# Performance work log

Hardware: AMD Instinct MI355X
Metric: run time of the kernel (lower is better)

## Reference

```python
import jax, jax.numpy as jnp
import numpy as np

EMB = 1024   # emb_dim
HID = 1024   # hid_dim (must equal EMB for the original router to be well-formed)
E = 16       # num_experts
K = 2        # num_active_experts


def setup_inputs() -> dict:
    key = jax.random.key(0)
    ks = jax.random.split(key, 5)
    s_in = (2.0 / EMB) ** 0.5
    s_hid = (2.0 / HID) ** 0.5
    x = jax.random.normal(ks[0], (2, 4096, EMB), dtype=jnp.float32)
    w_gate = jax.random.normal(ks[1], (EMB, E), dtype=jnp.float32) * s_in
    w1 = jax.random.normal(ks[2], (E, EMB, HID), dtype=jnp.float32) * s_in  # exp_1 weights
    w2 = jax.random.normal(ks[3], (E, EMB, HID), dtype=jnp.float32) * s_in  # exp_2 weights
    wc = jax.random.normal(ks[4], (E, HID, EMB), dtype=jnp.float32) * s_hid  # contr weights
    return {"x": x, "w_gate": w_gate, "w1": w1, "w2": w2, "wc": wc}


def reference(x, w_gate, w1, w2, wc):
    b, s, d = x.shape
    xf = x.reshape(-1, d)                      # [N, d]
    n = xf.shape[0]
    # Router: softmax over expert logits, then top-k (no renormalization of topk scores,
    # matching the torch module).
    probs = jax.nn.softmax(xf @ w_gate, axis=-1)   # [N, E]
    scores, idx = jax.lax.top_k(probs, K)          # [N, K]
    # Dense gate matrix: gate[t, e] = score if e in topk(t) else 0 (topk indices distinct).
    gates = jnp.zeros((n, E), dtype=xf.dtype).at[jnp.arange(n)[:, None], idx].set(scores)
    # Loop (scan) over the fixed expert count; each expert runs a SwiGLU MLP over all
    # tokens and its output is combined with the (mostly zero) gate weights. This is the
    # standard dense-combine MoE reference: same math as the masked torch loop since
    # unselected tokens get gate 0.
    def body(acc, ws):
        w1e, w2e, wce, ge = ws                 # [d,h], [d,h], [h,d], [N]
        h = jax.nn.silu(xf @ w1e) * (xf @ w2e)  # [N, h]
        return acc + ge[:, None] * (h @ wce), None

    out, _ = jax.lax.scan(body, jnp.zeros_like(xf), (w1, w2, wc, gates.T))
    return out.reshape(b, s, d)
```

## Files before the change

kernel.cpp:

```cpp
#include <hip/hip_runtime.h>
#include <hip/hip_bf16.h>
#include <stdint.h>

#define EMB 1024
#define HID 1024
#define NE 16
#define NTOK 8192
#define NSLOT (NTOK * 2)
#define BM 128
#define BN 128
#define BK 32

typedef __bf16 bf16;
typedef __bf16 bf16x8 __attribute__((ext_vector_type(8)));
typedef __bf16 bf16x4 __attribute__((ext_vector_type(4)));
typedef float f32x4 __attribute__((ext_vector_type(4)));

#define GLOAD16(g, l)                                                        \
  __builtin_amdgcn_global_load_lds(                                          \
      (const __attribute__((address_space(1))) void*)(g),                    \
      (__attribute__((address_space(3))) void*)(l), 16, 0, 0)

#define VMW(N) asm volatile("s_waitcnt vmcnt(" #N ")" ::: "memory")
#define NOPS ((void)0)

#define PH_PRE                                                \
  __builtin_amdgcn_s_barrier();                               \
  __builtin_amdgcn_s_setprio(1)
#define PH_POST                                               \
  __builtin_amdgcn_s_setprio(0);                              \
  __builtin_amdgcn_s_barrier()

#define LDA2(D, M, CK) (*(const bf16x8*)&sh[((((D)<<1) + wm) << 13) + l15 * 64 + (CK) + (M) * 1024])
#define LDB2(D, N, CK) (*(const bf16x8*)&sh[32768 + ((((D)<<1) + (wn >> 1)) << 13) + ((wn & 1) << 12) + l15 * 64 + (CK) + (N) * 1024])

#define STG2_A(D, KO) do {                                                    \
    GLOAD16(agp00 + (KO), (char*)sh + ((((D)<<1) + 0) << 14) + wb);           \
    GLOAD16(agp01 + (KO), (char*)sh + ((((D)<<1) + 0) << 14) + 8192 + wb);    \
    GLOAD16(agp10 + (KO), (char*)sh + ((((D)<<1) + 1) << 14) + wb);           \
    GLOAD16(agp11 + (KO), (char*)sh + ((((D)<<1) + 1) << 14) + 8192 + wb);    \
  } while (0)
#define STG2_B(D, KO) do {                                                    \
    GLOAD16(bgp00 + (KO), (char*)sh + 65536 + ((((D)<<1) + 0) << 14) + wb);   \
    GLOAD16(bgp01 + (KO), (char*)sh + 65536 + ((((D)<<1) + 0) << 14) + 8192 + wb); \
    GLOAD16(bgp10 + (KO), (char*)sh + 65536 + ((((D)<<1) + 1) << 14) + wb);   \
    GLOAD16(bgp11 + (KO), (char*)sh + 65536 + ((((D)<<1) + 1) << 14) + 8192 + wb); \
  } while (0)

#define MM(MB, FA, FB) do {                                                   \
    _Pragma("unroll") for (int mq = 0; mq < 4; mq++)                          \
    _Pragma("unroll") for (int nq = 0; nq < 4; nq++)                          \
      acc[(MB) + mq][nq] = __builtin_amdgcn_mfma_f32_16x16x32_bf16(           \
          (FA)[mq], (FB)[nq], acc[(MB) + mq][nq], 0, 0, 0);                   \
  } while (0)

#define KTILE2(D, S2, W2) do {                                                \
    bf16x8 a0[8], b0[4];                                                      \
    _Pragma("unroll") for (int q = 0; q < 4; q++) b0[q] = LDB2(D, q, c0);     \
    _Pragma("unroll") for (int q = 0; q < 8; q++) a0[q] = LDA2(D, q, c0);     \
    PH_PRE; MM(0, a0, b0); MM(4, a0 + 4, b0); PH_POST;                        \
    bf16x8 a1[8], b1[4];                                                      \
    _Pragma("unroll") for (int q = 0; q < 4; q++) b1[q] = LDB2(D, q, c1);     \
    _Pragma("unroll") for (int q = 0; q < 8; q++) a1[q] = LDA2(D, q, c1);     \
    S2; W2;                                                                   \
    PH_PRE; MM(0, a1, b1); MM(4, a1 + 4, b1); PH_POST;                        \
  } while (0)

#define KLOOP2(NT2) do {                                                      \
    STG2_A(0, 0); STG2_B(0, 0); STG2_A(1, 64); STG2_B(1, 64);                 \
    VMW(8); __builtin_amdgcn_s_barrier();                                     \
    _Pragma("unroll 1") for (int i = 0; i < (NT2) - 1; i++) {                 \
      int k2 = (i * 2 + 2) * 64, k3 = (i * 2 + 3) * 64;                       \
      KTILE2(0, { STG2_B(0, k2); STG2_A(0, k2); }, VMW(8));                   \
      KTILE2(1, { STG2_B(1, k3); STG2_A(1, k3); }, VMW(8));                   \
    }                                                                         \
    KTILE2(0, NOPS, VMW(0));                                                  \
    KTILE2(1, NOPS, NOPS);                                                    \
  } while (0)

__global__ void wgT_k(const float* __restrict__ wg, float* __restrict__ wgT) {
  int f = blockIdx.x * 256 + threadIdx.x;
  int d = f >> 4, e = f & 15;
  wgT[e * 1024 + d] = wg[f];
}

__launch_bounds__(512)
__global__ void prep_k(const float* __restrict__ w1, const float* __restrict__ w2,
                       const float* __restrict__ wcs, bf16* __restrict__ w1t,
                       bf16* __restrict__ w2t, bf16* __restrict__ wct,
                       const float* __restrict__ x, const float* __restrict__ wgT,
                       bf16* __restrict__ xb,
                       int* __restrict__ tokexp, float* __restrict__ tokgate) {
  __shared__ __align__(16) char lds[65536];
  int bid = blockIdx.x;
  if (bid < 6144) {
    typedef bf16 TileT[64][68];
    TileT* tile = (TileT*)lds;
    int half = threadIdx.x >> 8, t = threadIdx.x & 255;
    int u = bid * 2 + half;
    int zz = u >> 8, t16 = u & 255;
    int n0 = (t16 & 15) << 6, k0 = (t16 >> 4) << 6;
    const float* s; bf16* d;
    if (zz < 16)      { s = w1;  d = w1t; }
    else if (zz < 32) { s = w2;  d = w2t; }
    else              { s = wcs; d = wct; }
    int z = zz & 15;
    s += (size_t)z << 20;
    d += (size_t)z << 20;

    int r = t >> 4, c4 = t & 15;
#pragma unroll
    for (int i = 0; i < 4; i++) {
      int row = r + (i << 4);
      float4 v = *(const float4*)&s[(size_t)(k0 + row) * 1024 + n0 + (c4 << 2)];
      bf16x4 o;
      o[0] = (bf16)v.x; o[1] = (bf16)v.y; o[2] = (bf16)v.z; o[3] = (bf16)v.w;
      *(bf16x4*)&tile[half][row][c4 << 2] = o;
    }
    __syncthreads();

    int r8 = t >> 3, ch = t & 7;
#pragma unroll
    for (int i = 0; i < 2; i++) {
      int on = r8 + (i << 5);
      bf16x8 v;
#pragma unroll
      for (int j = 0; j < 8; j++) v[j] = tile[half][(ch << 3) + j][on];
      *(bf16x8*)&d[(size_t)(n0 + on) * 1024 + k0 + (ch << 3)] = v;
    }
  } else {
    float* wgs = (float*)lds;
    for (int i = threadIdx.x; i < 4096; i += 512)
      ((float4*)wgs)[i] = ((const float4*)wgT)[i];
    __syncthreads();

    int tok = (bid - 6144) * 8 + (threadIdx.x >> 6);
    int lane = threadIdx.x & 63;
    const float* xr = x + (size_t)tok * EMB;

    float acc[NE];
#pragma unroll
    for (int e = 0; e < NE; e++) acc[e] = 0.f;

#pragma unroll
    for (int c = 0; c < 4; c++) {
      float4 xv = ((const float4*)xr)[c * 64 + lane];
      int dbase = c * 256 + lane * 4;
      bf16x4 o;
      o[0] = (bf16)xv.x; o[1] = (bf16)xv.y; o[2] = (bf16)xv.z; o[3] = (bf16)xv.w;
      *(bf16x4*)(xb + (size_t)tok * EMB + dbase) = o;
#pragma unroll
      for (int e = 0; e < NE; e++) {
        float4 wv = *(const float4*)&wgs[e * 1024 + dbase];
        acc[e] += xv.x * wv.x + xv.y * wv.y + xv.z * wv.z + xv.w * wv.w;
      }
    }
#pragma unroll
    for (int e = 0; e < NE; e++) {
#pragma unroll
      for (int s2 = 32; s2 > 0; s2 >>= 1) acc[e] += __shfl_xor(acc[e], s2);
    }
    if (lane == 0) {
      float m = acc[0];
#pragma unroll
      for (int e = 1; e < NE; e++) m = fmaxf(m, acc[e]);
      float p[NE]; float sum = 0.f;
#pragma unroll
      for (int e = 0; e < NE; e++) { p[e] = __expf(acc[e] - m); sum += p[e]; }
      float inv = 1.f / sum;
#pragma unroll
      for (int e = 0; e < NE; e++) p[e] *= inv;
      int i1 = 0;
#pragma unroll
      for (int e = 1; e < NE; e++) if (p[e] > p[i1]) i1 = e;
      int i2 = (i1 == 0) ? 1 : 0;
#pragma unroll
      for (int e = 0; e < NE; e++) if (e != i1 && p[e] > p[i2]) i2 = e;
      tokexp[2 * tok] = i1; tokexp[2 * tok + 1] = i2;
      tokgate[2 * tok] = p[i1]; tokgate[2 * tok + 1] = p[i2];
    }
  }
}

__global__ void hist_k(const int* __restrict__ tokexp, int* __restrict__ blockcnt) {
  __shared__ int h[NE];
  int tid = threadIdx.x;
  if (tid < NE) h[tid] = 0;
  __syncthreads();
  int e = tokexp[blockIdx.x * 256 + tid];
  atomicAdd(&h[e], 1);
  __syncthreads();
  if (tid < NE) blockcnt[blockIdx.x * NE + tid] = h[tid];
}

__global__ void scan_k(const int* __restrict__ blockcnt, int* __restrict__ cnt,
                       int* __restrict__ eoff, int* __restrict__ blockoff) {
  __shared__ int scnt[NE], soff[NE];
  int t = threadIdx.x;
  if (t < NE) {
    int s = 0;
    for (int b = 0; b < 64; b++) s += blockcnt[b * NE + t];
    scnt[t] = s;
    cnt[t] = s;
  }
  __syncthreads();
  if (t == 0) {
    int s = 0;
    for (int e = 0; e < NE; e++) { soff[e] = s; eoff[e] = s; s += scnt[e]; }
  }
  __syncthreads();
  if (t < NE) {
    int run = soff[t];
    for (int b = 0; b < 64; b++) { blockoff[b * NE + t] = run; run += blockcnt[b * NE + t]; }
  }
}

__global__ void assign_k(const int* __restrict__ tokexp, const float* __restrict__ tokgate,
                         const int* __restrict__ blockoff, int* __restrict__ rowtok,
                         float* __restrict__ rowgate, int* __restrict__ posof) {
  __shared__ int wavecnt[4][NE];
  __shared__ int waveoff[4][NE];
  int tid = threadIdx.x;
  int w = tid >> 6, lane = tid & 63;
  int s = blockIdx.x * 256 + tid;
  int e = tokexp[s];
  int rank = 0;
  unsigned long long ltmask = (1ull << lane) - 1ull;
#pragma unroll
  for (int ee = 0; ee < NE; ee++) {
    unsigned long long bal = __ballot(e == ee);
    if (e == ee) rank = __popcll(bal & ltmask);
    if (lane == ee) wavecnt[w][ee] = __popcll(bal);
  }
  __syncthreads();
  if (tid < 64) {
    int ww = tid >> 4, ee = tid & 15;
    int off = 0;
    for (int p = 0; p < ww; p++) off += wavecnt[p][ee];
    waveoff[ww][ee] = off;
  }
  __syncthreads();
  int pos = blockoff[blockIdx.x * NE + e] + waveoff[w][e] + rank;
  rowtok[pos] = s >> 1;
  rowgate[pos] = tokgate[s];
  posof[s] = pos;
}

__launch_bounds__(256, 2)
__global__ void gemm1_k(const bf16* __restrict__ xb, const bf16* __restrict__ w1t,
                        const bf16* __restrict__ w2t, const int* __restrict__ cnt,
                        const int* __restrict__ eoff, const int* __restrict__ rowtok,
                        bf16* __restrict__ H) {
  int id = blockIdx.x;
  int nid = (id & 7) * 256 + (id >> 3);
  int e = nid >> 7;
  int rem = nid & 127;
  int m0 = (rem >> 3) * BM;
  int n0 = (rem & 7) * BN;
  int n_e = cnt[e];
  if (m0 >= n_e) return;
  int base = eoff[e];

  __shared__ __align__(16) bf16 sA[2][BM * BK];
  __shared__ __align__(16) bf16 sB1[2][BN * BK];
  __shared__ __align__(16) bf16 sB2[2][BN * BK];

  int tid = threadIdx.x;
  int lane = tid & 63;
  int w = tid >> 6;
  int wr = (w >> 1) << 6;
  int wc = (w & 1) << 6;

  int srow = tid >> 2;
  int kc = (((tid & 3) ^ ((tid >> 3) & 3)) << 3);

  const bf16 *ag0, *ag1;
  {
    int gi0 = base + m0 + srow;
    int gi1 = base + m0 + 64 + srow;
    gi0 = gi0 < NSLOT ? gi0 : NSLOT - 1;
    gi1 = gi1 < NSLOT ? gi1 : NSLOT - 1;
    ag0 = xb + (size_t)rowtok[gi0] * EMB + kc;
    ag1 = xb + (size_t)rowtok[gi1] * EMB + kc;
  }
  const bf16* b1g = w1t + ((size_t)e * HID + n0 + srow) * EMB + kc;
  const bf16* b2g = w2t + ((size_t)e * HID + n0 + srow) * EMB + kc;
  const size_t B64 = (size_t)64 * EMB;

  char* lA  = (char*)sA  + w * 1024;
  char* lB1 = (char*)sB1 + w * 1024;
  char* lB2 = (char*)sB2 + w * 1024;

#define G1STAGE(k0, b) do {                                                  \
    char* _A = lA + (b) * 8192; char* _B1 = lB1 + (b) * 8192;                \
    char* _B2 = lB2 + (b) * 8192;                                            \
    GLOAD16(ag0 + (k0), _A);                                                 \
    GLOAD16(ag1 + (k0), _A + 4096);                                          \
    GLOAD16(b1g + (k0), _B1);                                                \
    GLOAD16(b1g + B64 + (k0), _B1 + 4096);                                   \
    GLOAD16(b2g + (k0), _B2);                                                \
    GLOAD16(b2g + B64 + (k0), _B2 + 4096);                                   \
  } while (0)

  f32x4 acc1[4][4] = {};
  f32x4 acc2[4][4] = {};

  int chr = ((lane >> 4) ^ ((lane >> 1) & 3)) << 3;
  int ra = (wr + (lane & 15)) * BK + chr;
  int rb = (wc + (lane & 15)) * BK + chr;

  G1STAGE(0, 0);
  for (int t = 0; t < EMB / BK; t++) {
    int cur = t & 1;
    if (t < EMB / BK - 1) {
      G1STAGE((t + 1) * BK, cur ^ 1);
      VMW(6);
    } else {
      VMW(0);
    }
    __builtin_amdgcn_s_barrier();

    bf16x8 af[4], b1f[4], b2f[4];
#pragma unroll
    for (int m = 0; m < 4; m++) af[m] = *(const bf16x8*)&sA[cur][ra + m * 16 * BK];
#pragma unroll
    for (int n = 0; n < 4; n++) {
      b1f[n] = *(const bf16x8*)&sB1[cur][rb + n * 16 * BK];
      b2f[n] = *(const bf16x8*)&sB2[cur][rb + n * 16 * BK];
    }
#pragma unroll
    for (int m = 0; m < 4; m++)
#pragma unroll
      for (int n = 0; n < 4; n++) {
        acc1[m][n] = __builtin_amdgcn_mfma_f32_16x16x32_bf16(af[m], b1f[n], acc1[m][n], 0, 0, 0);
        acc2[m][n] = __builtin_amdgcn_mfma_f32_16x16x32_bf16(af[m], b2f[n], acc2[m][n], 0, 0, 0);
      }
    __builtin_amdgcn_s_barrier();
  }
#undef G1STAGE

  int rf = wr + ((lane >> 4) << 2);
  int cf = n0 + wc + (lane & 15);
#pragma unroll
  for (int m = 0; m < 4; m++) {
#pragma unroll
    for (int n = 0; n < 4; n++) {
#pragma unroll
      for (int b = 0; b < 4; b++) {
        int gr = m0 + rf + m * 16 + b;
        if (gr < n_e) {
          float c1 = acc1[m][n][b];
          float c2 = acc2[m][n][b];
          float h = c1 * c2 / (1.f + __expf(-c1));
          H[(size_t)(base + gr) * HID + cf + n * 16] = (bf16)h;
        }
      }
    }
  }
}

__launch_bounds__(512, 2)
__global__ void gemm2_k(const bf16* __restrict__ Hb, const bf16* __restrict__ wct,
                        const int* __restrict__ cnt, const int* __restrict__ eoff,
                        const float* __restrict__ rowgate, bf16* __restrict__ Ob) {
  int id = blockIdx.x;
  int nid = (id & 7) * 128 + (id >> 3);
  int e = nid >> 6, rem = nid & 63;
  int m0 = (rem >> 2) << 8;
  int n0 = (rem & 3) << 8;
  int n_e = cnt[e];
  if (m0 >= n_e) return;
  int base0 = eoff[e];
  extern __shared__ bf16 sh[];

  int tid = threadIdx.x, lane = tid & 63, w = tid >> 6;
  int wm = w >> 2, wn = w & 3;
  int l15 = lane & 15, l4 = lane >> 4, r7 = l15 & 7;
  int c0 = ((l4 ^ r7) << 3), c1 = (((4 + l4) ^ r7) << 3);
  int srow = tid >> 3;
  int kg8 = (((tid & 7) ^ (srow & 7)) << 3);
  int wb = w << 10;

  const bf16 *agp00, *agp01, *agp10, *agp11, *bgp00, *bgp01, *bgp10, *bgp11;
  {
    int g0 = base0 + m0 + srow;        g0 = g0 < NSLOT ? g0 : NSLOT - 1;
    int g1 = base0 + m0 + 64 + srow;   g1 = g1 < NSLOT ? g1 : NSLOT - 1;
    int g2 = base0 + m0 + 128 + srow;  g2 = g2 < NSLOT ? g2 : NSLOT - 1;
    int g3 = base0 + m0 + 192 + srow;  g3 = g3 < NSLOT ? g3 : NSLOT - 1;
    agp00 = Hb + ((size_t)g0 << 10) + kg8;
    agp01 = Hb + ((size_t)g1 << 10) + kg8;
    agp10 = Hb + ((size_t)g2 << 10) + kg8;
    agp11 = Hb + ((size_t)g3 << 10) + kg8;
    const bf16* wce = wct + ((size_t)e << 20);
    bgp00 = wce + ((size_t)(n0 + srow) << 10) + kg8;
    bgp01 = wce + ((size_t)(n0 + 64 + srow) << 10) + kg8;
    bgp10 = wce + ((size_t)(n0 + 128 + srow) << 10) + kg8;
    bgp11 = wce + ((size_t)(n0 + 192 + srow) << 10) + kg8;
  }

  f32x4 acc[8][4] = {};
  KLOOP2(8);

  int rb0 = m0 + (wm << 7) + (l4 << 2);
  int cb0 = n0 + (wn << 6) + l15;
#pragma unroll
  for (int m = 0; m < 8; m++)
#pragma unroll
    for (int b = 0; b < 4; b++) {
      int gr = rb0 + m * 16 + b;
      if (gr < n_e) {
        int idx = base0 + gr;
        float g = rowgate[idx];
        bf16* orow = Ob + ((size_t)idx << 10) + cb0;
#pragma unroll
        for (int n = 0; n < 4; n++)
          orow[n * 16] = (bf16)(g * acc[m][n][b]);
      }
    }
}

__global__ void combine_k(const bf16* __restrict__ Ob, const int* __restrict__ posof,
                          float* __restrict__ out) {
  int t = blockIdx.x;
  int c = threadIdx.x << 2;
  int p1 = posof[2 * t], p2 = posof[2 * t + 1];
  bf16x4 a = *(const bf16x4*)&Ob[((size_t)p1 << 10) + c];
  bf16x4 b = *(const bf16x4*)&Ob[((size_t)p2 << 10) + c];
  float4 o;
  o.x = (float)a[0] + (float)b[0];
  o.y = (float)a[1] + (float)b[1];
  o.z = (float)a[2] + (float)b[2];
  o.w = (float)a[3] + (float)b[3];
  *(float4*)&out[((size_t)t << 10) + c] = o;
}

extern "C" void kernel_launch(void* const* d_in, const int* in_sizes, int n_in,
                              void* d_out, int out_size, void* d_ws, size_t ws_size,
                              hipStream_t stream) {
  const float* x  = (const float*)d_in[0];
  const float* wg = (const float*)d_in[1];
  const float* w1 = (const float*)d_in[2];
  const float* w2 = (const float*)d_in[3];
  const float* wc = (const float*)d_in[4];
  float* out = (float*)d_out;

  const size_t WELEM = (size_t)NE << 20;
  bf16* w1t  = (bf16*)d_ws;
  bf16* w2t  = w1t + WELEM;
  bf16* wct  = w2t + WELEM;
  bf16* xb   = wct + WELEM;
  bf16* Hb   = xb + ((size_t)NTOK << 10);
  int* cnt      = (int*)(Hb + ((size_t)NSLOT << 10));
  int* eoff     = cnt + 16;
  int* blockcnt = eoff + 16;
  int* blockoff = blockcnt + 64 * 16;
  int* tokexp   = blockoff + 64 * 16;
  float* tokgate = (float*)(tokexp + NSLOT);
  int* rowtok    = (int*)(tokgate + NSLOT);
  float* rowgate = (float*)(rowtok + NSLOT);
  int* posof     = (int*)(rowgate + NSLOT);
  float* wgT     = (float*)(posof + NSLOT);
  bf16* Ob = w1t;

  hipFuncSetAttribute((const void*)gemm2_k, hipFuncAttributeMaxDynamicSharedMemorySize, 131072);

  wgT_k<<<64, 256, 0, stream>>>(wg, wgT);
  prep_k<<<7168, 512, 0, stream>>>(w1, w2, wc, w1t, w2t, wct, x, wgT, xb, tokexp, tokgate);
  hist_k<<<NSLOT / 256, 256, 0, stream>>>(tokexp, blockcnt);
  scan_k<<<1, 64, 0, stream>>>(blockcnt, cnt, eoff, blockoff);
  assign_k<<<NSLOT / 256, 256, 0, stream>>>(tokexp, tokgate, blockoff, rowtok, rowgate, posof);
  gemm1_k<<<2048, 256, 0, stream>>>(xb, w1t, w2t, cnt, eoff, rowtok, Hb);
  gemm2_k<<<1024, 512, 131072, stream>>>(Hb, wct, cnt, eoff, rowgate, Ob);
  combine_k<<<NTOK, 256, 0, stream>>>(Ob, posof, out);
}
```

Baseline: 273.0 us.

## Replace gemm2 256x256 pipelined kernel with simpler 256x128 double-buffered tile loop

Swaps the down-projection GEMM's 256x256 tile, 128KB dynamic-LDS, phase-scheduled K loop (setprio, paired K tiles) for a 256x128 tile using 48KB static LDS. It runs a plain double-buffered BK=32 loop with two barriers per step, and launch bounds rise to 4 blocks per CU. The aim is higher occupancy and less LDS per block. In exchange it gives up per-tile reuse, the prioritized MFMA scheduling and the deeper prefetch, and adds more barriers per unit of work.

```diff
diff --git a/kernel.cpp b/kernel.cpp
--- a/kernel.cpp
+++ b/kernel.cpp
@@ -22,61 +22,6 @@
       (__attribute__((address_space(3))) void*)(l), 16, 0, 0)
 
 #define VMW(N) asm volatile("s_waitcnt vmcnt(" #N ")" ::: "memory")
-#define NOPS ((void)0)
-
-#define PH_PRE                                                \
-  __builtin_amdgcn_s_barrier();                               \
-  __builtin_amdgcn_s_setprio(1)
-#define PH_POST                                               \
-  __builtin_amdgcn_s_setprio(0);                              \
-  __builtin_amdgcn_s_barrier()
-
-#define LDA2(D, M, CK) (*(const bf16x8*)&sh[((((D)<<1) + wm) << 13) + l15 * 64 + (CK) + (M) * 1024])
-#define LDB2(D, N, CK) (*(const bf16x8*)&sh[32768 + ((((D)<<1) + (wn >> 1)) << 13) + ((wn & 1) << 12) + l15 * 64 + (CK) + (N) * 1024])
-
-#define STG2_A(D, KO) do {                                                    \
-    GLOAD16(agp00 + (KO), (char*)sh + ((((D)<<1) + 0) << 14) + wb);           \
-    GLOAD16(agp01 + (KO), (char*)sh + ((((D)<<1) + 0) << 14) + 8192 + wb);    \
-    GLOAD16(agp10 + (KO), (char*)sh + ((((D)<<1) + 1) << 14) + wb);           \
-    GLOAD16(agp11 + (KO), (char*)sh + ((((D)<<1) + 1) << 14) + 8192 + wb);    \
-  } while (0)
-#define STG2_B(D, KO) do {                                                    \
-    GLOAD16(bgp00 + (KO), (char*)sh + 65536 + ((((D)<<1) + 0) << 14) + wb);   \
-    GLOAD16(bgp01 + (KO), (char*)sh + 65536 + ((((D)<<1) + 0) << 14) + 8192 + wb); \
-    GLOAD16(bgp10 + (KO), (char*)sh + 65536 + ((((D)<<1) + 1) << 14) + wb);   \
-    GLOAD16(bgp11 + (KO), (char*)sh + 65536 + ((((D)<<1) + 1) << 14) + 8192 + wb); \
-  } while (0)
-
-#define MM(MB, FA, FB) do {                                                   \
-    _Pragma("unroll") for (int mq = 0; mq < 4; mq++)                          \
-    _Pragma("unroll") for (int nq = 0; nq < 4; nq++)                          \
-      acc[(MB) + mq][nq] = __builtin_amdgcn_mfma_f32_16x16x32_bf16(           \
-          (FA)[mq], (FB)[nq], acc[(MB) + mq][nq], 0, 0, 0);                   \
-  } while (0)
-
-#define KTILE2(D, S2, W2) do {                                                \
-    bf16x8 a0[8], b0[4];                                                      \
-    _Pragma("unroll") for (int q = 0; q < 4; q++) b0[q] = LDB2(D, q, c0);     \
-    _Pragma("unroll") for (int q = 0; q < 8; q++) a0[q] = LDA2(D, q, c0);     \
-    PH_PRE; MM(0, a0, b0); MM(4, a0 + 4, b0); PH_POST;                        \
-    bf16x8 a1[8], b1[4];                                                      \
-    _Pragma("unroll") for (int q = 0; q < 4; q++) b1[q] = LDB2(D, q, c1);     \
-    _Pragma("unroll") for (int q = 0; q < 8; q++) a1[q] = LDA2(D, q, c1);     \
-    S2; W2;                                                                   \
-    PH_PRE; MM(0, a1, b1); MM(4, a1 + 4, b1); PH_POST;                        \
-  } while (0)
-
-#define KLOOP2(NT2) do {                                                      \
-    STG2_A(0, 0); STG2_B(0, 0); STG2_A(1, 64); STG2_B(1, 64);                 \
-    VMW(8); __builtin_amdgcn_s_barrier();                                     \
-    _Pragma("unroll 1") for (int i = 0; i < (NT2) - 1; i++) {                 \
-      int k2 = (i * 2 + 2) * 64, k3 = (i * 2 + 3) * 64;                       \
-      KTILE2(0, { STG2_B(0, k2); STG2_A(0, k2); }, VMW(8));                   \
-      KTILE2(1, { STG2_B(1, k3); STG2_A(1, k3); }, VMW(8));                   \
-    }                                                                         \
-    KTILE2(0, NOPS, VMW(0));                                                  \
-    KTILE2(1, NOPS, NOPS);                                                    \
-  } while (0)
 
 __global__ void wgT_k(const float* __restrict__ wg, float* __restrict__ wgT) {
   int f = blockIdx.x * 256 + threadIdx.x;
@@ -359,64 +304,100 @@
   }
 }
 
-__launch_bounds__(512, 2)
+__launch_bounds__(512, 4)
 __global__ void gemm2_k(const bf16* __restrict__ Hb, const bf16* __restrict__ wct,
                         const int* __restrict__ cnt, const int* __restrict__ eoff,
                         const float* __restrict__ rowgate, bf16* __restrict__ Ob) {
   int id = blockIdx.x;
   int nid = (id & 7) * 128 + (id >> 3);
   int e = nid >> 6, rem = nid & 63;
-  int m0 = (rem >> 2) << 8;
-  int n0 = (rem & 3) << 8;
+  int m0 = (rem >> 3) << 8;
+  int n0 = (rem & 7) << 7;
   int n_e = cnt[e];
   if (m0 >= n_e) return;
-  int base0 = eoff[e];
-  extern __shared__ bf16 sh[];
-
-  int tid = threadIdx.x, lane = tid & 63, w = tid >> 6;
-  int wm = w >> 2, wn = w & 3;
-  int l15 = lane & 15, l4 = lane >> 4, r7 = l15 & 7;
-  int c0 = ((l4 ^ r7) << 3), c1 = (((4 + l4) ^ r7) << 3);
-  int srow = tid >> 3;
-  int kg8 = (((tid & 7) ^ (srow & 7)) << 3);
-  int wb = w << 10;
-
-  const bf16 *agp00, *agp01, *agp10, *agp11, *bgp00, *bgp01, *bgp10, *bgp11;
+  int base = eoff[e];
+
+  __shared__ __align__(16) bf16 sA[2][256 * BK];
+  __shared__ __align__(16) bf16 sB[2][128 * BK];
+
+  int tid = threadIdx.x;
+  int lane = tid & 63;
+  int w = tid >> 6;
+  int wr = (w >> 1) << 6;
+  int wc = (w & 1) << 6;
+
+  int srow = tid >> 2;
+  int kc = (((tid & 3) ^ ((tid >> 3) & 3)) << 3);
+
+  const bf16 *ag0, *ag1;
   {
-    int g0 = base0 + m0 + srow;        g0 = g0 < NSLOT ? g0 : NSLOT - 1;
-    int g1 = base0 + m0 + 64 + srow;   g1 = g1 < NSLOT ? g1 : NSLOT - 1;
-    int g2 = base0 + m0 + 128 + srow;  g2 = g2 < NSLOT ? g2 : NSLOT - 1;
-    int g3 = base0 + m0 + 192 + srow;  g3 = g3 < NSLOT ? g3 : NSLOT - 1;
-    agp00 = Hb + ((size_t)g0 << 10) + kg8;
-    agp01 = Hb + ((size_t)g1 << 10) + kg8;
-    agp10 = Hb + ((size_t)g2 << 10) + kg8;
-    agp11 = Hb + ((size_t)g3 << 10) + kg8;
-    const bf16* wce = wct + ((size_t)e << 20);
-    bgp00 = wce + ((size_t)(n0 + srow) << 10) + kg8;
-    bgp01 = wce + ((size_t)(n0 + 64 + srow) << 10) + kg8;
-    bgp10 = wce + ((size_t)(n0 + 128 + srow) << 10) + kg8;
-    bgp11 = wce + ((size_t)(n0 + 192 + srow) << 10) + kg8;
-  }
-
-  f32x4 acc[8][4] = {};
-  KLOOP2(8);
-
-  int rb0 = m0 + (wm << 7) + (l4 << 2);
-  int cb0 = n0 + (wn << 6) + l15;
-#pragma unroll
-  for (int m = 0; m < 8; m++)
+    int gi0 = base + m0 + srow;
+    int gi1 = base + m0 + 128 + srow;
+    gi0 = gi0 < NSLOT ? gi0 : NSLOT - 1;
+    gi1 = gi1 < NSLOT ? gi1 : NSLOT - 1;
+    ag0 = Hb + ((size_t)gi0 << 10) + kc;
+    ag1 = Hb + ((size_t)gi1 << 10) + kc;
+  }
+  const bf16* bg = wct + ((size_t)e * EMB + n0 + srow) * HID + kc;
+
+  char* lA = (char*)sA + w * 1024;
+  char* lB = (char*)sB + w * 1024;
+
+#define G2STAGE(k0, b) do {                                                  \
+    char* _A = lA + (b) * 16384; char* _B = lB + (b) * 8192;                 \
+    GLOAD16(ag0 + (k0), _A);                                                 \
+    GLOAD16(ag1 + (k0), _A + 8192);                                          \
+    GLOAD16(bg + (k0), _B);                                                  \
+  } while (0)
+
+  f32x4 acc[4][4] = {};
+
+  int chr = ((lane >> 4) ^ ((lane >> 1) & 3)) << 3;
+  int ra = (wr + (lane & 15)) * BK + chr;
+  int rb = (wc + (lane & 15)) * BK + chr;
+
+  G2STAGE(0, 0);
+  for (int t = 0; t < HID / BK; t++) {
+    int cur = t & 1;
+    if (t < HID / BK - 1) {
+      G2STAGE((t + 1) * BK, cur ^ 1);
+      VMW(3);
+    } else {
+      VMW(0);
+    }
+    __builtin_amdgcn_s_barrier();
+
+    bf16x8 af[4], bfr[4];
+#pragma unroll
+    for (int m = 0; m < 4; m++) af[m] = *(const bf16x8*)&sA[cur][ra + m * 16 * BK];
+#pragma unroll
+    for (int n = 0; n < 4; n++) bfr[n] = *(const bf16x8*)&sB[cur][rb + n * 16 * BK];
+#pragma unroll
+    for (int m = 0; m < 4; m++)
+#pragma unroll
+      for (int n = 0; n < 4; n++)
+        acc[m][n] = __builtin_amdgcn_mfma_f32_16x16x32_bf16(af[m], bfr[n], acc[m][n], 0, 0, 0);
+    __builtin_amdgcn_s_barrier();
+  }
+#undef G2STAGE
+
+  int rf = wr + ((lane >> 4) << 2);
+  int cf = n0 + wc + (lane & 15);
+#pragma unroll
+  for (int m = 0; m < 4; m++) {
 #pragma unroll
     for (int b = 0; b < 4; b++) {
-      int gr = rb0 + m * 16 + b;
+      int gr = m0 + rf + m * 16 + b;
       if (gr < n_e) {
-        int idx = base0 + gr;
+        int idx = base + gr;
         float g = rowgate[idx];
-        bf16* orow = Ob + ((size_t)idx << 10) + cb0;
+        bf16* orow = Ob + ((size_t)idx << 10) + cf;
 #pragma unroll
         for (int n = 0; n < 4; n++)
           orow[n * 16] = (bf16)(g * acc[m][n][b]);
       }
     }
+  }
 }
 
 __global__ void combine_k(const bf16* __restrict__ Ob, const int* __restrict__ posof,
@@ -462,14 +443,12 @@
   float* wgT     = (float*)(posof + NSLOT);
   bf16* Ob = w1t;
 
-  hipFuncSetAttribute((const void*)gemm2_k, hipFuncAttributeMaxDynamicSharedMemorySize, 131072);
-
   wgT_k<<<64, 256, 0, stream>>>(wg, wgT);
   prep_k<<<7168, 512, 0, stream>>>(w1, w2, wc, w1t, w2t, wct, x, wgT, xb, tokexp, tokgate);
   hist_k<<<NSLOT / 256, 256, 0, stream>>>(tokexp, blockcnt);
   scan_k<<<1, 64, 0, stream>>>(blockcnt, cnt, eoff, blockoff);
   assign_k<<<NSLOT / 256, 256, 0, stream>>>(tokexp, tokgate, blockoff, rowtok, rowgate, posof);
   gemm1_k<<<2048, 256, 0, stream>>>(xb, w1t, w2t, cnt, eoff, rowtok, Hb);
-  gemm2_k<<<1024, 512, 131072, stream>>>(Hb, wct, cnt, eoff, rowgate, Ob);
+  gemm2_k<<<1024, 512, 0, stream>>>(Hb, wct, cnt, eoff, rowgate, Ob);
   combine_k<<<NTOK, 256, 0, stream>>>(Ob, posof, out);
 }
```

After: 267.2 us. 1.02x faster.
